# Optimization experiments

Hardware: AMD Instinct MI355X
Metric: run time of the kernel (lower is better)

Reference implementation:

```python
import jax, jax.numpy as jnp
import numpy as np

N_NODES = 100000
N_EDGES = 1600000
HID = 64
N_LAYERS = 3
BN_EPS = 1e-5


def setup_inputs() -> dict:
    key = jax.random.key(0)
    ks = jax.random.split(key, 10)
    x = jax.random.normal(ks[0], (N_NODES, HID), dtype=jnp.float32)
    edge_index = jax.random.randint(ks[1], (2, N_EDGES), 0, N_NODES, dtype=jnp.int64)
    edge_atten = jax.random.uniform(ks[2], (N_EDGES, 1), dtype=jnp.float32)
    s = 1.0 / np.sqrt(HID)
    W1 = jax.random.normal(ks[3], (N_LAYERS, HID, HID), dtype=jnp.float32) * s
    b1 = jax.random.normal(ks[4], (N_LAYERS, HID), dtype=jnp.float32) * s
    gamma = jnp.ones((N_LAYERS, HID), dtype=jnp.float32)
    beta = jnp.zeros((N_LAYERS, HID), dtype=jnp.float32)
    W2 = jax.random.normal(ks[5], (N_LAYERS, HID, HID), dtype=jnp.float32) * s
    b2 = jax.random.normal(ks[6], (N_LAYERS, HID), dtype=jnp.float32) * s
    return {"x": x, "edge_index": edge_index, "edge_atten": edge_atten,
            "W1": W1, "b1": b1, "gamma": gamma, "beta": beta, "W2": W2, "b2": b2}


def reference(x, edge_index, edge_atten, W1, b1, gamma, beta, W2, b2):
    # GIN with GINConv (eps=0): out = nn(sum_{j->i} x_j * edge_atten + x_i), then ReLU
    src = edge_index[0]  # x_j gathered from source nodes
    dst = edge_index[1]  # scatter-add into target nodes
    n = x.shape[0]
    for i in range(N_LAYERS):
        msg = x[src] * edge_atten                                   # [E, H]
        agg = jax.ops.segment_sum(msg, dst, num_segments=n)         # [N, H]
        h = agg + x                                                 # (1 + eps)*x_r, eps=0
        # MLP: Linear -> BatchNorm1d (training mode, batch stats) -> ReLU -> Linear
        h = h @ W1[i] + b1[i]
        mu = jnp.mean(h, axis=0)
        var = jnp.var(h, axis=0)
        h = (h - mu) * jax.lax.rsqrt(var + BN_EPS) * gamma[i] + beta[i]
        h = jax.nn.relu(h)
        h = h @ W2[i] + b2[i]
        x = jax.nn.relu(h)  # outer self.relu after each conv
    return x
```

## Files before the change

### kernel.cpp

```cpp
#include <hip/hip_runtime.h>

#define NN 100000
#define NE 1600000
#define HID 64
#define CH 32
#define NT (NN / 16)
#define NL 3
#define BN_EPS 1e-5f
#define BSH 7
#define BNODES 128
#define NB 782
#define GP 16
#define BIN_CHUNK 8192
#define BIN_GRID ((NE + BIN_CHUNK - 1) / BIN_CHUNK)

typedef __attribute__((ext_vector_type(8))) short short8;
typedef __attribute__((ext_vector_type(4))) float f32x4;

__device__ __forceinline__ float bf2f(unsigned short u) {
    union { unsigned int i; float f; } v; v.i = ((unsigned int)u) << 16; return v.f;
}
__device__ __forceinline__ unsigned short f2bf(float f) {
    union { float f; unsigned int i; } v; v.f = f;
    unsigned int r = v.i + 0x7FFFu + ((v.i >> 16) & 1u);
    return (unsigned short)(r >> 16);
}

__global__ void k_conv(const float* __restrict__ x, ushort* __restrict__ xc) {
    int i = blockIdx.x * blockDim.x + threadIdx.x;
    float4 v = ((const float4*)x)[i];
    int node = i >> 4, c4 = (i & 15) * 4;
    int q = c4 >> 5, m = c4 & 31;
    ushort4 o;
    o.x = f2bf(v.x); o.y = f2bf(v.y); o.z = f2bf(v.z); o.w = f2bf(v.w);
    *(ushort4*)(xc + (size_t)q * NN * CH + (size_t)node * CH + m) = o;
}

__global__ void k_wpack(const float* __restrict__ W1, const float* __restrict__ W2,
                        ushort* __restrict__ wf) {
    int s = blockIdx.x, l = threadIdx.x;
    int layer = s >> 2, kind = s & 3;
    const float* W = ((kind < 2) ? W1 : W2) + (size_t)layer * HID * HID;
    ushort* o = wf + (size_t)s * 4096;
    for (int kh = 0; kh < 2; ++kh)
        for (int t = 0; t < 4; ++t)
            for (int j = 0; j < 8; ++j) {
                int k = kh * 32 + (l >> 4) * 8 + j;
                int n = t * 16 + (l & 15);
                float f = W[k * HID + n];
                ushort hi = f2bf(f);
                o[((kh * 4 + t) * 64 + l) * 8 + j] =
                    (kind & 1) ? f2bf(f - bf2f(hi)) : hi;
            }
}

__global__ __launch_bounds__(1024) void k_histB(const int* __restrict__ dst,
                                                int* __restrict__ ghist) {
    __shared__ int lh[NB];
    int tid = threadIdx.x;
    for (int i = tid; i < NB; i += 1024) lh[i] = 0;
    __syncthreads();
    int base = blockIdx.x * BIN_CHUNK;
    int end = min(base + BIN_CHUNK, NE);
    for (int e = base + tid * 4; e + 3 < end; e += 4096) {
        int4 d = *(const int4*)(dst + e);
        atomicAdd(&lh[d.x >> BSH], 1);
        atomicAdd(&lh[d.y >> BSH], 1);
        atomicAdd(&lh[d.z >> BSH], 1);
        atomicAdd(&lh[d.w >> BSH], 1);
    }
    __syncthreads();
    for (int i = tid; i < NB; i += 1024)
        if (lh[i]) atomicAdd(&ghist[i * GP], lh[i]);
}

__global__ void k_scanB(const int* __restrict__ ghist, int* __restrict__ boffB,
                        int* __restrict__ gcur) {
    __shared__ int t[1024];
    int tid = threadIdx.x;
    int v = (tid < NB) ? ghist[tid * GP] : 0;
    t[tid] = v;
    __syncthreads();
    for (int d = 1; d < 1024; d <<= 1) {
        int u = (tid >= d) ? t[tid - d] : 0;
        __syncthreads();
        t[tid] += u;
        __syncthreads();
    }
    if (tid < NB) { int ex = t[tid] - v; boffB[tid] = ex; gcur[tid * GP] = ex; }
    if (tid == 0) boffB[NB] = NE;
}

__global__ __launch_bounds__(1024) void k_binB(const int* __restrict__ ei,
                                               const float* __restrict__ att,
                                               int* __restrict__ gcur,
                                               int2* __restrict__ evb) {
    __shared__ int lh[NB];
    int tid = threadIdx.x;
    for (int i = tid; i < NB; i += 1024) lh[i] = 0;
    __syncthreads();
    int base = blockIdx.x * BIN_CHUNK;
    int end = min(base + BIN_CHUNK, NE);
    for (int e = base + tid * 4; e + 3 < end; e += 4096) {
        int4 d = *(const int4*)(ei + NE + e);
        atomicAdd(&lh[d.x >> BSH], 1);
        atomicAdd(&lh[d.y >> BSH], 1);
        atomicAdd(&lh[d.z >> BSH], 1);
        atomicAdd(&lh[d.w >> BSH], 1);
    }
    __syncthreads();
    for (int i = tid; i < NB; i += 1024) {
        int c = lh[i];
        lh[i] = c ? atomicAdd(&gcur[i * GP], c) : 0;
    }
    __syncthreads();
    for (int e = base + tid * 4; e + 3 < end; e += 4096) {
        int4 s = *(const int4*)(ei + e);
        int4 d = *(const int4*)(ei + NE + e);
        float4 a = *(const float4*)(att + e);
        int p0 = atomicAdd(&lh[d.x >> BSH], 1);
        int p1 = atomicAdd(&lh[d.y >> BSH], 1);
        int p2 = atomicAdd(&lh[d.z >> BSH], 1);
        int p3 = atomicAdd(&lh[d.w >> BSH], 1);
        evb[p0] = make_int2(s.x | ((d.x & (BNODES - 1)) << 17), __float_as_int(a.x));
        evb[p1] = make_int2(s.y | ((d.y & (BNODES - 1)) << 17), __float_as_int(a.y));
        evb[p2] = make_int2(s.z | ((d.z & (BNODES - 1)) << 17), __float_as_int(a.z));
        evb[p3] = make_int2(s.w | ((d.w & (BNODES - 1)) << 17), __float_as_int(a.w));
    }
}

__global__ __launch_bounds__(256) void k_scatter2(const int2* __restrict__ evb,
                                                  const int* __restrict__ boffB,
                                                  int* __restrict__ offs,
                                                  uint* __restrict__ evc) {
    __shared__ int h[BNODES];
    __shared__ int cur[BNODES];
    int tid = threadIdx.x;
    int b = blockIdx.x;
    int node0 = b << BSH;
    int nvalid = min(BNODES, NN - node0);
    int e0 = boffB[b], e1 = boffB[b + 1];
    if (tid < BNODES) h[tid] = 0;
    __syncthreads();
    for (int e = e0 + tid * 2; e < e1; e += 512) {
        int2 r0 = evb[e];
        int v1 = (e + 1 < e1);
        int2 r1 = evb[v1 ? e + 1 : e];
        atomicAdd(&h[r0.x >> 17], 1);
        if (v1) atomicAdd(&h[r1.x >> 17], 1);
    }
    __syncthreads();
    int v = (tid < BNODES) ? h[tid] : 0;
    for (int d = 1; d < BNODES; d <<= 1) {
        int u = (tid >= d && tid < BNODES) ? h[tid - d] : 0;
        __syncthreads();
        if (tid < BNODES) h[tid] += u;
        __syncthreads();
    }
    if (tid < BNODES) {
        int start = e0 + h[tid] - v;
        cur[tid] = start;
        if (tid < nvalid) offs[node0 + tid] = start;
    }
    if (b == NB - 1 && tid == 0) offs[NN] = NE;
    __syncthreads();
    for (int e = e0 + tid * 2; e < e1; e += 512) {
        int2 r0 = evb[e];
        int v1 = (e + 1 < e1);
        int2 r1 = evb[v1 ? e + 1 : e];
        int p0 = atomicAdd(&cur[r0.x >> 17], 1);
        int p1 = v1 ? atomicAdd(&cur[r1.x >> 17], 1) : 0;
        uint a0 = (uint)(__int_as_float(r0.y) * 32767.0f + 0.5f);
        evc[p0] = ((uint)r0.x & 0x1FFFFu) | (a0 << 17);
        if (v1) {
            uint a1 = (uint)(__int_as_float(r1.y) * 32767.0f + 0.5f);
            evc[p1] = ((uint)r1.x & 0x1FFFFu) | (a1 << 17);
        }
    }
}

__global__ __launch_bounds__(256, 8) void k_gather(const ushort* __restrict__ xc,
                                                   const int* __restrict__ offs,
                                                   const uint* __restrict__ evc,
                                                   ushort* __restrict__ aggc) {
    int tid = threadIdx.x;
    int wv = tid >> 6, lane = tid & 63;
    int g = lane >> 4;
    int c2 = lane & 15;
    int q = (blockIdx.x & 7) >> 2;
    int wb = ((blockIdx.x >> 3) << 2) | (blockIdx.x & 3);
    const ushort* xq = xc + (size_t)q * NN * CH + c2 * 2;
    ushort* aq = aggc + (size_t)q * NN * CH;
    int slot = wb * 4 + wv;
    for (int base = slot * 8; base < NN; base += 4096 * 8) {
        uint self0 = *(const uint*)(xq + (base + g) * CH);
        uint self1 = *(const uint*)(xq + (base + g + 4) * CH);
        int myoff = offs[min(base + c2, NN)];
        float rx0 = 0.f, ry0 = 0.f, rx1 = 0.f, ry1 = 0.f;
        int e0n = __shfl(myoff, 0, 64);
        int e1n = __shfl(myoff, 1, 64);
        uint evj = evc[min(e0n + g, max(e1n - 1, 0))];
        for (int j = 0; j < 8; ++j) {
            int e0 = e0n, e1 = e1n;
            uint evu = evj;
            if (j < 7) {
                e0n = __shfl(myoff, j + 1, 64);
                e1n = __shfl(myoff, j + 2, 64);
                evj = evc[min(e0n + g, max(e1n - 1, 0))];
            }
            int e1m1 = max(e1 - 1, 0);
            float ax = 0.f, ay = 0.f;
            for (int e = e0; e < e1; e += 4) {
                uint evn = evc[min(e + 4 + g, e1m1)];
                float a = (e + g < e1) ? (float)(evu >> 17) * (1.0f / 32767.0f) : 0.f;
                uint r = *(const uint*)(xq + (evu & 0x1FFFF) * CH);
                union { uint u; float f; } lo, hi;
                lo.u = r << 16; hi.u = r & 0xFFFF0000u;
                ax += lo.f * a; ay += hi.f * a;
                evu = evn;
            }
            ax += __shfl_xor(ax, 16, 64); ax += __shfl_xor(ax, 32, 64);
            ay += __shfl_xor(ay, 16, 64); ay += __shfl_xor(ay, 32, 64);
            if (j == g)     { rx0 = ax; ry0 = ay; }
            if (j == g + 4) { rx1 = ax; ry1 = ay; }
        }
        union { uint u; float f; } s;
        s.u = self0 << 16;         rx0 += s.f;
        s.u = self0 & 0xFFFF0000u; ry0 += s.f;
        s.u = self1 << 16;         rx1 += s.f;
        s.u = self1 & 0xFFFF0000u; ry1 += s.f;
        uint o0 = ((uint)f2bf(rx0)) | (((uint)f2bf(ry0)) << 16);
        uint o1 = ((uint)f2bf(rx1)) | (((uint)f2bf(ry1)) << 16);
        *(uint*)(aq + (base + g) * CH + c2 * 2) = o0;
        *(uint*)(aq + (base + g + 4) * CH + c2 * 2) = o1;
    }
}

__global__ __launch_bounds__(256, 2) void k_mlp1(const ushort* __restrict__ aggc,
                                                 const ushort* __restrict__ wfb,
                                                 const float* __restrict__ b1,
                                                 ushort* __restrict__ h,
                                                 float* __restrict__ stats) {
    __shared__ float red1[4][64], red2[4][64];
    int tid = threadIdx.x, wv = tid >> 6, l = tid & 63;
    int lg = l >> 4, lc = l & 15;
    short8 bhi[2][4], blo[2][4];
#pragma unroll
    for (int kh = 0; kh < 2; ++kh)
#pragma unroll
        for (int t = 0; t < 4; ++t) {
            bhi[kh][t] = *(const short8*)(wfb + ((kh * 4 + t) * 64 + l) * 8);
            blo[kh][t] = *(const short8*)(wfb + 4096 + ((kh * 4 + t) * 64 + l) * 8);
        }
    f32x4 bias4[4];
#pragma unroll
    for (int t = 0; t < 4; ++t) {
        float4 bv = *(const float4*)(b1 + t * 16 + lg * 4);
        bias4[t] = (f32x4){bv.x, bv.y, bv.z, bv.w};
    }
    float s1[16], s2[16];
#pragma unroll
    for (int i = 0; i < 16; ++i) { s1[i] = 0.f; s2[i] = 0.f; }
    int gw = blockIdx.x * 4 + wv, nw = gridDim.x * 4;
    for (int tile = gw; tile < NT; tile += nw) {
        int node = tile * 16 + lc;
        const ushort* ap = aggc + (size_t)node * CH + lg * 8;
        short8 a0 = *(const short8*)ap;
        short8 a1 = *(const short8*)(ap + (size_t)NN * CH);
        f32x4 acc[4];
#pragma unroll
        for (int t = 0; t < 4; ++t) {
            acc[t] = bias4[t];
            acc[t] = __builtin_amdgcn_mfma_f32_16x16x32_bf16(bhi[0][t], a0, acc[t], 0, 0, 0);
            acc[t] = __builtin_amdgcn_mfma_f32_16x16x32_bf16(bhi[1][t], a1, acc[t], 0, 0, 0);
            acc[t] = __builtin_amdgcn_mfma_f32_16x16x32_bf16(blo[0][t], a0, acc[t], 0, 0, 0);
            acc[t] = __builtin_amdgcn_mfma_f32_16x16x32_bf16(blo[1][t], a1, acc[t], 0, 0, 0);
        }
#pragma unroll
        for (int t = 0; t < 4; ++t) {
            ushort4 o;
            float d0 = acc[t][0], d1 = acc[t][1], d2 = acc[t][2], d3 = acc[t][3];
            s1[t * 4 + 0] += d0; s2[t * 4 + 0] += d0 * d0;
            s1[t * 4 + 1] += d1; s2[t * 4 + 1] += d1 * d1;
            s1[t * 4 + 2] += d2; s2[t * 4 + 2] += d2 * d2;
            s1[t * 4 + 3] += d3; s2[t * 4 + 3] += d3 * d3;
            o.x = f2bf(d0); o.y = f2bf(d1); o.z = f2bf(d2); o.w = f2bf(d3);
            *(ushort4*)(h + (size_t)(t >> 1) * NN * CH + (size_t)node * CH
                        + (t & 1) * 16 + lg * 4) = o;
        }
    }
#pragma unroll
    for (int i = 0; i < 16; ++i) {
        s1[i] += __shfl_xor(s1[i], 1, 64); s1[i] += __shfl_xor(s1[i], 2, 64);
        s1[i] += __shfl_xor(s1[i], 4, 64); s1[i] += __shfl_xor(s1[i], 8, 64);
        s2[i] += __shfl_xor(s2[i], 1, 64); s2[i] += __shfl_xor(s2[i], 2, 64);
        s2[i] += __shfl_xor(s2[i], 4, 64); s2[i] += __shfl_xor(s2[i], 8, 64);
    }
    if (lc == 0) {
#pragma unroll
        for (int t = 0; t < 4; ++t)
#pragma unroll
            for (int r = 0; r < 4; ++r) {
                red1[wv][t * 16 + lg * 4 + r] = s1[t * 4 + r];
                red2[wv][t * 16 + lg * 4 + r] = s2[t * 4 + r];
            }
    }
    __syncthreads();
    if (tid < 64)
        atomicAdd(&stats[tid], red1[0][tid] + red1[1][tid] + red1[2][tid] + red1[3][tid]);
    else if (tid < 128) {
        int c = tid - 64;
        atomicAdd(&stats[HID + c], red2[0][c] + red2[1][c] + red2[2][c] + red2[3][c]);
    }
}

__global__ __launch_bounds__(256, 2) void k_mlp2(const ushort* __restrict__ wfb,
                                                 const float* __restrict__ b2,
                                                 const float* __restrict__ gamma,
                                                 const float* __restrict__ beta,
                                                 const float* __restrict__ stats,
                                                 const ushort* __restrict__ h,
                                                 ushort* __restrict__ xc_out,
                                                 float* __restrict__ f_out,
                                                 int write_f32) {
    int tid = threadIdx.x, wv = tid >> 6, l = tid & 63;
    int lg = l >> 4, lc = l & 15;
    short8 bhi[2][4], blo[2][4];
#pragma unroll
    for (int kh = 0; kh < 2; ++kh)
#pragma unroll
        for (int t = 0; t < 4; ++t) {
            bhi[kh][t] = *(const short8*)(wfb + 8192 + ((kh * 4 + t) * 64 + l) * 8);
            blo[kh][t] = *(const short8*)(wfb + 12288 + ((kh * 4 + t) * 64 + l) * 8);
        }
    f32x4 bias4[4];
#pragma unroll
    for (int t = 0; t < 4; ++t) {
        float4 bv = *(const float4*)(b2 + t * 16 + lg * 4);
        bias4[t] = (f32x4){bv.x, bv.y, bv.z, bv.w};
    }
    float aCk[2][8], bCk[2][8];
#pragma unroll
    for (int kh = 0; kh < 2; ++kh)
#pragma unroll
        for (int j = 0; j < 8; ++j) {
            int k = kh * 32 + lg * 8 + j;
            float mu = stats[k] * (1.0f / NN);
            float var = fmaxf(stats[HID + k] * (1.0f / NN) - mu * mu, 0.f);
            float aC = gamma[k] * rsqrtf(var + BN_EPS);
            aCk[kh][j] = aC;
            bCk[kh][j] = beta[k] - mu * aC;
        }
    int gw = blockIdx.x * 4 + wv, nw = gridDim.x * 4;
    for (int tile = gw; tile < NT; tile += nw) {
        int node = tile * 16 + lc;
        const ushort* hp = h + (size_t)node * CH + lg * 8;
        short8 a0r = *(const short8*)hp;
        short8 a1r = *(const short8*)(hp + (size_t)NN * CH);
        short8 a0, a1;
#pragma unroll
        for (int j = 0; j < 8; ++j) {
            float v0 = fmaxf(aCk[0][j] * bf2f((ushort)a0r[j]) + bCk[0][j], 0.f);
            float v1 = fmaxf(aCk[1][j] * bf2f((ushort)a1r[j]) + bCk[1][j], 0.f);
            a0[j] = (short)f2bf(v0);
            a1[j] = (short)f2bf(v1);
        }
        f32x4 acc[4];
#pragma unroll
        for (int t = 0; t < 4; ++t) {
            acc[t] = bias4[t];
            acc[t] = __builtin_amdgcn_mfma_f32_16x16x32_bf16(bhi[0][t], a0, acc[t], 0, 0, 0);
            acc[t] = __builtin_amdgcn_mfma_f32_16x16x32_bf16(bhi[1][t], a1, acc[t], 0, 0, 0);
            acc[t] = __builtin_amdgcn_mfma_f32_16x16x32_bf16(blo[0][t], a0, acc[t], 0, 0, 0);
            acc[t] = __builtin_amdgcn_mfma_f32_16x16x32_bf16(blo[1][t], a1, acc[t], 0, 0, 0);
        }
        if (write_f32) {
#pragma unroll
            for (int t = 0; t < 4; ++t) {
                float4 o4;
                o4.x = fmaxf(acc[t][0], 0.f); o4.y = fmaxf(acc[t][1], 0.f);
                o4.z = fmaxf(acc[t][2], 0.f); o4.w = fmaxf(acc[t][3], 0.f);
                *(float4*)(f_out + (size_t)node * HID + t * 16 + lg * 4) = o4;
            }
        } else {
#pragma unroll
            for (int t = 0; t < 4; ++t) {
                ushort4 o;
                o.x = f2bf(fmaxf(acc[t][0], 0.f)); o.y = f2bf(fmaxf(acc[t][1], 0.f));
                o.z = f2bf(fmaxf(acc[t][2], 0.f)); o.w = f2bf(fmaxf(acc[t][3], 0.f));
                *(ushort4*)(xc_out + (size_t)(t >> 1) * NN * CH + (size_t)node * CH
                            + (t & 1) * 16 + lg * 4) = o;
            }
        }
    }
}

extern "C" void kernel_launch(void* const* d_in, const int* in_sizes, int n_in,
                              void* d_out, int out_size, void* d_ws, size_t ws_size,
                              hipStream_t stream) {
    const float* x_in  = (const float*)d_in[0];
    const int*   ei    = (const int*)d_in[1];
    const float* att   = (const float*)d_in[2];
    const float* W1    = (const float*)d_in[3];
    const float* b1    = (const float*)d_in[4];
    const float* gamma = (const float*)d_in[5];
    const float* beta  = (const float*)d_in[6];
    const float* W2    = (const float*)d_in[7];
    const float* b2    = (const float*)d_in[8];
    float* out = (float*)d_out;

    char* ws = (char*)d_ws;
    size_t off = 0;
    auto alloc = [&](size_t bytes) -> void* {
        void* p = ws + off;
        off += (bytes + 255) & ~(size_t)255;
        return p;
    };
    ushort* xc    = (ushort*)alloc((size_t)NN * HID * 2);
    ushort* aggc  = (ushort*)alloc((size_t)NN * HID * 2);
    ushort* hb    = (ushort*)alloc((size_t)NN * HID * 2);
    ushort* wf    = (ushort*)alloc((size_t)12 * 4096 * 2);
    int*    ghist = (int*)alloc((size_t)NB * GP * 4);
    int*    boffB = (int*)alloc((size_t)(NB + 1) * 4);
    int*    gcur  = (int*)alloc((size_t)NB * GP * 4);
    int*    offs  = (int*)alloc((size_t)(NN + 1) * 4);
    int2*   evb   = (int2*)alloc((size_t)NE * 8);
    uint*   evc   = (uint*)alloc((size_t)NE * 4);
    float*  stats = (float*)alloc(NL * 128 * 4);

    hipMemsetAsync(ghist, 0, (size_t)NB * GP * 4, stream);
    hipMemsetAsync(stats, 0, NL * 128 * 4, stream);

    k_conv<<<(NN * HID / 4 + 255) / 256, 256, 0, stream>>>(x_in, xc);
    k_wpack<<<12, 64, 0, stream>>>(W1, W2, wf);
    k_histB<<<BIN_GRID, 1024, 0, stream>>>(ei + NE, ghist);
    k_scanB<<<1, 1024, 0, stream>>>(ghist, boffB, gcur);
    k_binB<<<BIN_GRID, 1024, 0, stream>>>(ei, att, gcur, evb);
    k_scatter2<<<NB, 256, 0, stream>>>(evb, boffB, offs, evc);

    for (int l = 0; l < NL; ++l) {
        const ushort* wfb = wf + (size_t)l * 4 * 4096;
        k_gather<<<2048, 256, 0, stream>>>(xc, offs, evc, aggc);
        k_mlp1<<<1024, 256, 0, stream>>>(aggc, wfb, b1 + l * HID, hb, stats + l * 128);
        k_mlp2<<<1024, 256, 0, stream>>>(wfb, b2 + l * HID,
                                         gamma + l * HID, beta + l * HID,
                                         stats + l * 128, hb,
                                         xc, out, (l == NL - 1) ? 1 : 0);
    }
}
```

Baseline: 391.1 us.

## Switch to row-major bf16 features and sub-sort edges by source range in gather

Drops the two-half channel-split feature layout in favour of plain row-major 64-channel bf16 rows, updating both MLP kernels to match. The scatter stage now also sub-buckets each destination's edges into eight source-index ranges, which gives sorted gather locality, and writes a finer offset table. The gather kernel is rewritten so each half-wave handles one full node row (32 lanes × 2 channels), three nodes per wave, with a 4-way unrolled edge loop instead of the shuffle-based 8-node scheme. This aims to improve L2 locality of the random source reads and remove shuffle overhead. The cost is a larger offset table and more per-key loop overhead for small segments.

Result: slower. 529.2 us (+35.3%).

```diff
diff --git a/kernel.cpp b/kernel.cpp
--- a/kernel.cpp
+++ b/kernel.cpp
@@ -3,16 +3,21 @@
 #define NN 100000
 #define NE 1600000
 #define HID 64
-#define CH 32
 #define NT (NN / 16)
 #define NL 3
 #define BN_EPS 1e-5f
 #define BSH 7
 #define BNODES 128
 #define NB 782
+#define NSH 8
+#define SSH 14
+#define NKEY (BNODES * NSH)
 #define GP 16
 #define BIN_CHUNK 8192
 #define BIN_GRID ((NE + BIN_CHUNK - 1) / BIN_CHUNK)
+#define GBLK 4167
+#define GW_TOT (GBLK * 4)
+#define NPAIR (NN / 2)
 
 typedef __attribute__((ext_vector_type(8))) short short8;
 typedef __attribute__((ext_vector_type(4))) float f32x4;
@@ -25,15 +30,19 @@
     unsigned int r = v.i + 0x7FFFu + ((v.i >> 16) & 1u);
     return (unsigned short)(r >> 16);
 }
-
-__global__ void k_conv(const float* __restrict__ x, ushort* __restrict__ xc) {
+__device__ __forceinline__ float lof(uint r) {
+    union { uint u; float f; } v; v.u = r << 16; return v.f;
+}
+__device__ __forceinline__ float hif(uint r) {
+    union { uint u; float f; } v; v.u = r & 0xFFFF0000u; return v.f;
+}
+
+__global__ void k_conv(const float* __restrict__ x, ushort* __restrict__ xb) {
     int i = blockIdx.x * blockDim.x + threadIdx.x;
     float4 v = ((const float4*)x)[i];
-    int node = i >> 4, c4 = (i & 15) * 4;
-    int q = c4 >> 5, m = c4 & 31;
     ushort4 o;
     o.x = f2bf(v.x); o.y = f2bf(v.y); o.z = f2bf(v.z); o.w = f2bf(v.w);
-    *(ushort4*)(xc + (size_t)q * NN * CH + (size_t)node * CH + m) = o;
+    ((ushort4*)xb)[i] = o;
 }
 
 __global__ void k_wpack(const float* __restrict__ W1, const float* __restrict__ W2,
@@ -131,109 +140,112 @@
 
 __global__ __launch_bounds__(256) void k_scatter2(const int2* __restrict__ evb,
                                                   const int* __restrict__ boffB,
-                                                  int* __restrict__ offs,
+                                                  int* __restrict__ offs2,
                                                   uint* __restrict__ evc) {
-    __shared__ int h[BNODES];
-    __shared__ int cur[BNODES];
-    int tid = threadIdx.x;
-    int b = blockIdx.x;
+    __shared__ int h[NKEY];
+    __shared__ int cur[NKEY];
+    __shared__ int tsum[256];
+    int tid = threadIdx.x, b = blockIdx.x;
     int node0 = b << BSH;
-    int nvalid = min(BNODES, NN - node0);
     int e0 = boffB[b], e1 = boffB[b + 1];
-    if (tid < BNODES) h[tid] = 0;
+    for (int i = tid; i < NKEY; i += 256) h[i] = 0;
     __syncthreads();
     for (int e = e0 + tid * 2; e < e1; e += 512) {
         int2 r0 = evb[e];
-        int v1 = (e + 1 < e1);
-        int2 r1 = evb[v1 ? e + 1 : e];
-        atomicAdd(&h[r0.x >> 17], 1);
-        if (v1) atomicAdd(&h[r1.x >> 17], 1);
-    }
-    __syncthreads();
-    int v = (tid < BNODES) ? h[tid] : 0;
-    for (int d = 1; d < BNODES; d <<= 1) {
-        int u = (tid >= d && tid < BNODES) ? h[tid - d] : 0;
+        atomicAdd(&h[((r0.x >> 17) << 3) | ((r0.x & 0x1FFFF) >> SSH)], 1);
+        if (e + 1 < e1) {
+            int2 r1 = evb[e + 1];
+            atomicAdd(&h[((r1.x >> 17) << 3) | ((r1.x & 0x1FFFF) >> SSH)], 1);
+        }
+    }
+    __syncthreads();
+    int c0 = h[tid * 4], c1 = h[tid * 4 + 1], c2 = h[tid * 4 + 2], c3 = h[tid * 4 + 3];
+    int S = c0 + c1 + c2 + c3;
+    tsum[tid] = S;
+    __syncthreads();
+    for (int d = 1; d < 256; d <<= 1) {
+        int u = (tid >= d) ? tsum[tid - d] : 0;
         __syncthreads();
-        if (tid < BNODES) h[tid] += u;
+        tsum[tid] += u;
         __syncthreads();
     }
-    if (tid < BNODES) {
-        int start = e0 + h[tid] - v;
-        cur[tid] = start;
-        if (tid < nvalid) offs[node0 + tid] = start;
-    }
-    if (b == NB - 1 && tid == 0) offs[NN] = NE;
+    int st0 = e0 + tsum[tid] - S;
+    int st1 = st0 + c0, st2 = st1 + c1, st3 = st2 + c2;
+    cur[tid * 4] = st0; cur[tid * 4 + 1] = st1;
+    cur[tid * 4 + 2] = st2; cur[tid * 4 + 3] = st3;
+    int gk = node0 * NSH + tid * 4;
+    offs2[gk] = st0; offs2[gk + 1] = st1; offs2[gk + 2] = st2; offs2[gk + 3] = st3;
+    if (b == NB - 1 && tid == 0) offs2[(size_t)NB * BNODES * NSH] = NE;
     __syncthreads();
     for (int e = e0 + tid * 2; e < e1; e += 512) {
         int2 r0 = evb[e];
-        int v1 = (e + 1 < e1);
-        int2 r1 = evb[v1 ? e + 1 : e];
-        int p0 = atomicAdd(&cur[r0.x >> 17], 1);
-        int p1 = v1 ? atomicAdd(&cur[r1.x >> 17], 1) : 0;
+        int k0 = ((r0.x >> 17) << 3) | ((r0.x & 0x1FFFF) >> SSH);
+        int p0 = atomicAdd(&cur[k0], 1);
         uint a0 = (uint)(__int_as_float(r0.y) * 32767.0f + 0.5f);
         evc[p0] = ((uint)r0.x & 0x1FFFFu) | (a0 << 17);
-        if (v1) {
+        if (e + 1 < e1) {
+            int2 r1 = evb[e + 1];
+            int k1 = ((r1.x >> 17) << 3) | ((r1.x & 0x1FFFF) >> SSH);
+            int p1 = atomicAdd(&cur[k1], 1);
             uint a1 = (uint)(__int_as_float(r1.y) * 32767.0f + 0.5f);
             evc[p1] = ((uint)r1.x & 0x1FFFFu) | (a1 << 17);
         }
     }
 }
 
-__global__ __launch_bounds__(256, 8) void k_gather(const ushort* __restrict__ xc,
-                                                   const int* __restrict__ offs,
+#define EDGE_BODY(AX, AY) \
+    for (; e + 4 <= e1; e += 4) { \
+        uint w0 = evc[e], w1 = evc[e + 1], w2 = evc[e + 2], w3 = evc[e + 3]; \
+        uint r0 = xq[(w0 & 0x1FFFF) * 32 + hl]; \
+        uint r1 = xq[(w1 & 0x1FFFF) * 32 + hl]; \
+        uint r2 = xq[(w2 & 0x1FFFF) * 32 + hl]; \
+        uint r3 = xq[(w3 & 0x1FFFF) * 32 + hl]; \
+        float a0 = (float)(w0 >> 17) * (1.0f / 32767.0f); \
+        float a1 = (float)(w1 >> 17) * (1.0f / 32767.0f); \
+        float a2 = (float)(w2 >> 17) * (1.0f / 32767.0f); \
+        float a3 = (float)(w3 >> 17) * (1.0f / 32767.0f); \
+        AX += lof(r0) * a0 + lof(r1) * a1 + lof(r2) * a2 + lof(r3) * a3; \
+        AY += hif(r0) * a0 + hif(r1) * a1 + hif(r2) * a2 + hif(r3) * a3; \
+    } \
+    for (; e < e1; ++e) { \
+        uint w = evc[e]; \
+        uint r = xq[(w & 0x1FFFF) * 32 + hl]; \
+        float a = (float)(w >> 17) * (1.0f / 32767.0f); \
+        AX += lof(r) * a; \
+        AY += hif(r) * a; \
+    }
+
+__global__ __launch_bounds__(256, 8) void k_gather(const ushort* __restrict__ xb,
+                                                   const int* __restrict__ offs2,
                                                    const uint* __restrict__ evc,
-                                                   ushort* __restrict__ aggc) {
+                                                   ushort* __restrict__ agg) {
     int tid = threadIdx.x;
-    int wv = tid >> 6, lane = tid & 63;
-    int g = lane >> 4;
-    int c2 = lane & 15;
-    int q = (blockIdx.x & 7) >> 2;
-    int wb = ((blockIdx.x >> 3) << 2) | (blockIdx.x & 3);
-    const ushort* xq = xc + (size_t)q * NN * CH + c2 * 2;
-    ushort* aq = aggc + (size_t)q * NN * CH;
-    int slot = wb * 4 + wv;
-    for (int base = slot * 8; base < NN; base += 4096 * 8) {
-        uint self0 = *(const uint*)(xq + (base + g) * CH);
-        uint self1 = *(const uint*)(xq + (base + g + 4) * CH);
-        int myoff = offs[min(base + c2, NN)];
-        float rx0 = 0.f, ry0 = 0.f, rx1 = 0.f, ry1 = 0.f;
-        int e0n = __shfl(myoff, 0, 64);
-        int e1n = __shfl(myoff, 1, 64);
-        uint evj = evc[min(e0n + g, max(e1n - 1, 0))];
-        for (int j = 0; j < 8; ++j) {
-            int e0 = e0n, e1 = e1n;
-            uint evu = evj;
-            if (j < 7) {
-                e0n = __shfl(myoff, j + 1, 64);
-                e1n = __shfl(myoff, j + 2, 64);
-                evj = evc[min(e0n + g, max(e1n - 1, 0))];
-            }
-            int e1m1 = max(e1 - 1, 0);
-            float ax = 0.f, ay = 0.f;
-            for (int e = e0; e < e1; e += 4) {
-                uint evn = evc[min(e + 4 + g, e1m1)];
-                float a = (e + g < e1) ? (float)(evu >> 17) * (1.0f / 32767.0f) : 0.f;
-                uint r = *(const uint*)(xq + (evu & 0x1FFFF) * CH);
-                union { uint u; float f; } lo, hi;
-                lo.u = r << 16; hi.u = r & 0xFFFF0000u;
-                ax += lo.f * a; ay += hi.f * a;
-                evu = evn;
-            }
-            ax += __shfl_xor(ax, 16, 64); ax += __shfl_xor(ax, 32, 64);
-            ay += __shfl_xor(ay, 16, 64); ay += __shfl_xor(ay, 32, 64);
-            if (j == g)     { rx0 = ax; ry0 = ay; }
-            if (j == g + 4) { rx1 = ax; ry1 = ay; }
-        }
-        union { uint u; float f; } s;
-        s.u = self0 << 16;         rx0 += s.f;
-        s.u = self0 & 0xFFFF0000u; ry0 += s.f;
-        s.u = self1 << 16;         rx1 += s.f;
-        s.u = self1 & 0xFFFF0000u; ry1 += s.f;
-        uint o0 = ((uint)f2bf(rx0)) | (((uint)f2bf(ry0)) << 16);
-        uint o1 = ((uint)f2bf(rx1)) | (((uint)f2bf(ry1)) << 16);
-        *(uint*)(aq + (base + g) * CH + c2 * 2) = o0;
-        *(uint*)(aq + (base + g + 4) * CH + c2 * 2) = o1;
-    }
+    int gw = blockIdx.x * 4 + (tid >> 6);
+    int lane = tid & 63;
+    int half = lane >> 5, hl = lane & 31;
+    const uint* xq = (const uint*)xb;
+    int p0 = gw, p1 = GW_TOT + gw, p2 = 2 * GW_TOT + gw;
+    bool v2 = (p2 < NPAIR);
+    int n0 = p0 * 2 + half;
+    int n1 = p1 * 2 + half;
+    int n2 = min(p2 * 2 + half, NN - 1);
+    uint sr;
+    sr = xq[n0 * 32 + hl]; float ax0 = lof(sr), ay0 = hif(sr);
+    sr = xq[n1 * 32 + hl]; float ax1 = lof(sr), ay1 = hif(sr);
+    sr = xq[n2 * 32 + hl]; float ax2 = lof(sr), ay2 = hif(sr);
+    for (int s = 0; s < NSH; ++s) {
+        int key, e0, e1, e;
+        key = n0 * NSH + s; e0 = offs2[key]; e1 = offs2[key + 1]; e = e0;
+        EDGE_BODY(ax0, ay0)
+        key = n1 * NSH + s; e0 = offs2[key]; e1 = offs2[key + 1]; e = e0;
+        EDGE_BODY(ax1, ay1)
+        key = n2 * NSH + s; e0 = offs2[key]; e1 = offs2[key + 1]; e = e0;
+        EDGE_BODY(ax2, ay2)
+    }
+    uint* ag = (uint*)agg;
+    ag[n0 * 32 + hl] = ((uint)f2bf(ax0)) | (((uint)f2bf(ay0)) << 16);
+    ag[n1 * 32 + hl] = ((uint)f2bf(ax1)) | (((uint)f2bf(ay1)) << 16);
+    if (v2) ag[n2 * 32 + hl] = ((uint)f2bf(ax2)) | (((uint)f2bf(ay2)) << 16);
 }
 
 __global__ __launch_bounds__(256, 2) void k_mlp1(const ushort* __restrict__ aggc,
@@ -264,9 +276,9 @@
     int gw = blockIdx.x * 4 + wv, nw = gridDim.x * 4;
     for (int tile = gw; tile < NT; tile += nw) {
         int node = tile * 16 + lc;
-        const ushort* ap = aggc + (size_t)node * CH + lg * 8;
+        const ushort* ap = aggc + (size_t)node * HID + lg * 8;
         short8 a0 = *(const short8*)ap;
-        short8 a1 = *(const short8*)(ap + (size_t)NN * CH);
+        short8 a1 = *(const short8*)(ap + 32);
         f32x4 acc[4];
 #pragma unroll
         for (int t = 0; t < 4; ++t) {
@@ -285,8 +297,7 @@
             s1[t * 4 + 2] += d2; s2[t * 4 + 2] += d2 * d2;
             s1[t * 4 + 3] += d3; s2[t * 4 + 3] += d3 * d3;
             o.x = f2bf(d0); o.y = f2bf(d1); o.z = f2bf(d2); o.w = f2bf(d3);
-            *(ushort4*)(h + (size_t)(t >> 1) * NN * CH + (size_t)node * CH
-                        + (t & 1) * 16 + lg * 4) = o;
+            *(ushort4*)(h + (size_t)node * HID + t * 16 + lg * 4) = o;
         }
     }
 #pragma unroll
@@ -320,7 +331,7 @@
                                                  const float* __restrict__ beta,
                                                  const float* __restrict__ stats,
                                                  const ushort* __restrict__ h,
-                                                 ushort* __restrict__ xc_out,
+                                                 ushort* __restrict__ xb_out,
                                                  float* __restrict__ f_out,
                                                  int write_f32) {
     int tid = threadIdx.x, wv = tid >> 6, l = tid & 63;
@@ -354,9 +365,9 @@
     int gw = blockIdx.x * 4 + wv, nw = gridDim.x * 4;
     for (int tile = gw; tile < NT; tile += nw) {
         int node = tile * 16 + lc;
-        const ushort* hp = h + (size_t)node * CH + lg * 8;
+        const ushort* hp = h + (size_t)node * HID + lg * 8;
         short8 a0r = *(const short8*)hp;
-        short8 a1r = *(const short8*)(hp + (size_t)NN * CH);
+        short8 a1r = *(const short8*)(hp + 32);
         short8 a0, a1;
 #pragma unroll
         for (int j = 0; j < 8; ++j) {
@@ -388,8 +399,7 @@
                 ushort4 o;
                 o.x = f2bf(fmaxf(acc[t][0], 0.f)); o.y = f2bf(fmaxf(acc[t][1], 0.f));
                 o.z = f2bf(fmaxf(acc[t][2], 0.f)); o.w = f2bf(fmaxf(acc[t][3], 0.f));
-                *(ushort4*)(xc_out + (size_t)(t >> 1) * NN * CH + (size_t)node * CH
-                            + (t & 1) * 16 + lg * 4) = o;
+                *(ushort4*)(xb_out + (size_t)node * HID + t * 16 + lg * 4) = o;
             }
         }
     }
@@ -416,14 +426,14 @@
         off += (bytes + 255) & ~(size_t)255;
         return p;
     };
-    ushort* xc    = (ushort*)alloc((size_t)NN * HID * 2);
-    ushort* aggc  = (ushort*)alloc((size_t)NN * HID * 2);
+    ushort* xb    = (ushort*)alloc((size_t)NN * HID * 2);
+    ushort* aggb  = (ushort*)alloc((size_t)NN * HID * 2);
     ushort* hb    = (ushort*)alloc((size_t)NN * HID * 2);
     ushort* wf    = (ushort*)alloc((size_t)12 * 4096 * 2);
     int*    ghist = (int*)alloc((size_t)NB * GP * 4);
     int*    boffB = (int*)alloc((size_t)(NB + 1) * 4);
     int*    gcur  = (int*)alloc((size_t)NB * GP * 4);
-    int*    offs  = (int*)alloc((size_t)(NN + 1) * 4);
+    int*    offs2 = (int*)alloc(((size_t)NB * BNODES * NSH + 16) * 4);
     int2*   evb   = (int2*)alloc((size_t)NE * 8);
     uint*   evc   = (uint*)alloc((size_t)NE * 4);
     float*  stats = (float*)alloc(NL * 128 * 4);
@@ -431,20 +441,20 @@
     hipMemsetAsync(ghist, 0, (size_t)NB * GP * 4, stream);
     hipMemsetAsync(stats, 0, NL * 128 * 4, stream);
 
-    k_conv<<<(NN * HID / 4 + 255) / 256, 256, 0, stream>>>(x_in, xc);
+    k_conv<<<(NN * HID / 4 + 255) / 256, 256, 0, stream>>>(x_in, xb);
     k_wpack<<<12, 64, 0, stream>>>(W1, W2, wf);
     k_histB<<<BIN_GRID, 1024, 0, stream>>>(ei + NE, ghist);
     k_scanB<<<1, 1024, 0, stream>>>(ghist, boffB, gcur);
     k_binB<<<BIN_GRID, 1024, 0, stream>>>(ei, att, gcur, evb);
-    k_scatter2<<<NB, 256, 0, stream>>>(evb, boffB, offs, evc);
+    k_scatter2<<<NB, 256, 0, stream>>>(evb, boffB, offs2, evc);
 
     for (int l = 0; l < NL; ++l) {
         const ushort* wfb = wf + (size_t)l * 4 * 4096;
-        k_gather<<<2048, 256, 0, stream>>>(xc, offs, evc, aggc);
-        k_mlp1<<<1024, 256, 0, stream>>>(aggc, wfb, b1 + l * HID, hb, stats + l * 128);
+        k_gather<<<GBLK, 256, 0, stream>>>(xb, offs2, evc, aggb);
+        k_mlp1<<<1024, 256, 0, stream>>>(aggb, wfb, b1 + l * HID, hb, stats + l * 128);
         k_mlp2<<<1024, 256, 0, stream>>>(wfb, b2 + l * HID,
                                          gamma + l * HID, beta + l * HID,
                                          stats + l * 128, hb,
-                                         xc, out, (l == NL - 1) ? 1 : 0);
-    }
-}
+                                         xb, out, (l == NL - 1) ? 1 : 0);
+    }
+}
```

## Sort nodes by degree and gather full 128B rows with wave-wide edge fetch

Applied to the files above, without the earlier changes.

Adds a counting sort of nodes by in-degree (histogram, scan, place) so each wave of the gather handles eight nodes of similar degree, which cuts divergence in the per-node edge loops. The feature layout changes from two 32-channel planes to a contiguous 64-channel bf16 row, and each lane now loads a uint4 (8 channels), so one neighbor costs a single 128-byte row fetch. Edge words are loaded once per 8 edges and shared across lanes with ds_bpermute. The cost is three extra setup kernels plus a perm indirection, and a fixed grid of 3125 blocks that assumes NN is a multiple of 32.

Result: faster. 332.6 us (-15.0%).

```diff
diff --git a/kernel.cpp b/kernel.cpp
--- a/kernel.cpp
+++ b/kernel.cpp
@@ -3,7 +3,6 @@
 #define NN 100000
 #define NE 1600000
 #define HID 64
-#define CH 32
 #define NT (NN / 16)
 #define NL 3
 #define BN_EPS 1e-5f
@@ -13,6 +12,9 @@
 #define GP 16
 #define BIN_CHUNK 8192
 #define BIN_GRID ((NE + BIN_CHUNK - 1) / BIN_CHUNK)
+#define GBLK 3125
+#define DCHUNK 8192
+#define DGRID ((NN + DCHUNK - 1) / DCHUNK)
 
 typedef __attribute__((ext_vector_type(8))) short short8;
 typedef __attribute__((ext_vector_type(4))) float f32x4;
@@ -25,15 +27,19 @@
     unsigned int r = v.i + 0x7FFFu + ((v.i >> 16) & 1u);
     return (unsigned short)(r >> 16);
 }
-
-__global__ void k_conv(const float* __restrict__ x, ushort* __restrict__ xc) {
+__device__ __forceinline__ float lof(uint r) {
+    union { uint u; float f; } v; v.u = r << 16; return v.f;
+}
+__device__ __forceinline__ float hif(uint r) {
+    union { uint u; float f; } v; v.u = r & 0xFFFF0000u; return v.f;
+}
+
+__global__ void k_conv(const float* __restrict__ x, ushort* __restrict__ xb) {
     int i = blockIdx.x * blockDim.x + threadIdx.x;
     float4 v = ((const float4*)x)[i];
-    int node = i >> 4, c4 = (i & 15) * 4;
-    int q = c4 >> 5, m = c4 & 31;
     ushort4 o;
     o.x = f2bf(v.x); o.y = f2bf(v.y); o.z = f2bf(v.z); o.w = f2bf(v.w);
-    *(ushort4*)(xc + (size_t)q * NN * CH + (size_t)node * CH + m) = o;
+    ((ushort4*)xb)[i] = o;
 }
 
 __global__ void k_wpack(const float* __restrict__ W1, const float* __restrict__ W2,
@@ -179,61 +185,108 @@
     }
 }
 
-__global__ __launch_bounds__(256, 8) void k_gather(const ushort* __restrict__ xc,
+__global__ __launch_bounds__(1024) void k_dhist(const int* __restrict__ offs,
+                                                int* __restrict__ dh) {
+    __shared__ int lh[256];
+    int tid = threadIdx.x;
+    if (tid < 256) lh[tid] = 0;
+    __syncthreads();
+    int lo = blockIdx.x * DCHUNK, hi = min(lo + DCHUNK, NN);
+    for (int i = lo + tid; i < hi; i += 1024)
+        atomicAdd(&lh[min(offs[i + 1] - offs[i], 255)], 1);
+    __syncthreads();
+    if (tid < 256 && lh[tid]) atomicAdd(&dh[tid * GP], lh[tid]);
+}
+
+__global__ void k_dscan(const int* __restrict__ dh, int* __restrict__ dcur) {
+    __shared__ int t[256];
+    int tid = threadIdx.x;
+    int v = dh[tid * GP];
+    t[tid] = v;
+    __syncthreads();
+    for (int d = 1; d < 256; d <<= 1) {
+        int u = (tid >= d) ? t[tid - d] : 0;
+        __syncthreads();
+        t[tid] += u;
+        __syncthreads();
+    }
+    dcur[tid * GP] = t[tid] - v;
+}
+
+__global__ __launch_bounds__(1024) void k_dplace(const int* __restrict__ offs,
+                                                 int* __restrict__ dcur,
+                                                 int* __restrict__ perm) {
+    __shared__ int lh[256];
+    __shared__ int lbase[256];
+    int tid = threadIdx.x;
+    if (tid < 256) lh[tid] = 0;
+    __syncthreads();
+    int lo = blockIdx.x * DCHUNK, hi = min(lo + DCHUNK, NN);
+    int mybin[8], myrk[8];
+#pragma unroll 8
+    for (int u = 0; u < 8; ++u) {
+        int i = lo + u * 1024 + tid;
+        if (i < hi) {
+            int b = min(offs[i + 1] - offs[i], 255);
+            mybin[u] = b;
+            myrk[u] = atomicAdd(&lh[b], 1);
+        } else mybin[u] = -1;
+    }
+    __syncthreads();
+    if (tid < 256) {
+        int c = lh[tid];
+        lbase[tid] = c ? atomicAdd(&dcur[tid * GP], c) : 0;
+    }
+    __syncthreads();
+#pragma unroll 8
+    for (int u = 0; u < 8; ++u) {
+        int i = lo + u * 1024 + tid;
+        if (mybin[u] >= 0) perm[lbase[mybin[u]] + myrk[u]] = i;
+    }
+}
+
+__global__ __launch_bounds__(256, 4) void k_gather(const ushort* __restrict__ xb,
                                                    const int* __restrict__ offs,
                                                    const uint* __restrict__ evc,
-                                                   ushort* __restrict__ aggc) {
-    int tid = threadIdx.x;
-    int wv = tid >> 6, lane = tid & 63;
-    int g = lane >> 4;
-    int c2 = lane & 15;
-    int q = (blockIdx.x & 7) >> 2;
-    int wb = ((blockIdx.x >> 3) << 2) | (blockIdx.x & 3);
-    const ushort* xq = xc + (size_t)q * NN * CH + c2 * 2;
-    ushort* aq = aggc + (size_t)q * NN * CH;
-    int slot = wb * 4 + wv;
-    for (int base = slot * 8; base < NN; base += 4096 * 8) {
-        uint self0 = *(const uint*)(xq + (base + g) * CH);
-        uint self1 = *(const uint*)(xq + (base + g + 4) * CH);
-        int myoff = offs[min(base + c2, NN)];
-        float rx0 = 0.f, ry0 = 0.f, rx1 = 0.f, ry1 = 0.f;
-        int e0n = __shfl(myoff, 0, 64);
-        int e1n = __shfl(myoff, 1, 64);
-        uint evj = evc[min(e0n + g, max(e1n - 1, 0))];
+                                                   const int* __restrict__ perm,
+                                                   ushort* __restrict__ agg) {
+    int tid = threadIdx.x;
+    int wid = blockIdx.x * 4 + (tid >> 6);
+    int lane = tid & 63;
+    int g = lane >> 3, k = lane & 7;
+    const uint4* xq4 = (const uint4*)xb;
+    uint4* aq4 = (uint4*)agg;
+    int node = perm[wid * 8 + g];
+    int e0 = offs[node], e1 = offs[node + 1];
+    int deg = e1 - e0;
+    uint4 s4 = xq4[(size_t)node * 8 + k];
+    float ax0 = lof(s4.x), ay0 = hif(s4.x);
+    float ax1 = lof(s4.y), ay1 = hif(s4.y);
+    float ax2 = lof(s4.z), ay2 = hif(s4.z);
+    float ax3 = lof(s4.w), ay3 = hif(s4.w);
+    int maxd = deg;
+    maxd = max(maxd, __shfl_xor(maxd, 8, 64));
+    maxd = max(maxd, __shfl_xor(maxd, 16, 64));
+    maxd = max(maxd, __shfl_xor(maxd, 32, 64));
+    for (int base = 0; base < maxd; base += 8) {
+        uint ew = evc[min(e0 + base + k, NE - 1)];
+#pragma unroll 8
         for (int j = 0; j < 8; ++j) {
-            int e0 = e0n, e1 = e1n;
-            uint evu = evj;
-            if (j < 7) {
-                e0n = __shfl(myoff, j + 1, 64);
-                e1n = __shfl(myoff, j + 2, 64);
-                evj = evc[min(e0n + g, max(e1n - 1, 0))];
-            }
-            int e1m1 = max(e1 - 1, 0);
-            float ax = 0.f, ay = 0.f;
-            for (int e = e0; e < e1; e += 4) {
-                uint evn = evc[min(e + 4 + g, e1m1)];
-                float a = (e + g < e1) ? (float)(evu >> 17) * (1.0f / 32767.0f) : 0.f;
-                uint r = *(const uint*)(xq + (evu & 0x1FFFF) * CH);
-                union { uint u; float f; } lo, hi;
-                lo.u = r << 16; hi.u = r & 0xFFFF0000u;
-                ax += lo.f * a; ay += hi.f * a;
-                evu = evn;
-            }
-            ax += __shfl_xor(ax, 16, 64); ax += __shfl_xor(ax, 32, 64);
-            ay += __shfl_xor(ay, 16, 64); ay += __shfl_xor(ay, 32, 64);
-            if (j == g)     { rx0 = ax; ry0 = ay; }
-            if (j == g + 4) { rx1 = ax; ry1 = ay; }
-        }
-        union { uint u; float f; } s;
-        s.u = self0 << 16;         rx0 += s.f;
-        s.u = self0 & 0xFFFF0000u; ry0 += s.f;
-        s.u = self1 << 16;         rx1 += s.f;
-        s.u = self1 & 0xFFFF0000u; ry1 += s.f;
-        uint o0 = ((uint)f2bf(rx0)) | (((uint)f2bf(ry0)) << 16);
-        uint o1 = ((uint)f2bf(rx1)) | (((uint)f2bf(ry1)) << 16);
-        *(uint*)(aq + (base + g) * CH + c2 * 2) = o0;
-        *(uint*)(aq + (base + g + 4) * CH + c2 * 2) = o1;
-    }
+            uint w = (uint)__builtin_amdgcn_ds_bpermute((g * 8 + j) << 2, (int)ew);
+            float a = (base + j < deg) ? (float)(w >> 17) * (1.0f / 32767.0f) : 0.f;
+            uint4 r = xq4[(size_t)(w & 0x1FFFF) * 8 + k];
+            ax0 += lof(r.x) * a; ay0 += hif(r.x) * a;
+            ax1 += lof(r.y) * a; ay1 += hif(r.y) * a;
+            ax2 += lof(r.z) * a; ay2 += hif(r.z) * a;
+            ax3 += lof(r.w) * a; ay3 += hif(r.w) * a;
+        }
+    }
+    uint4 o;
+    o.x = ((uint)f2bf(ax0)) | (((uint)f2bf(ay0)) << 16);
+    o.y = ((uint)f2bf(ax1)) | (((uint)f2bf(ay1)) << 16);
+    o.z = ((uint)f2bf(ax2)) | (((uint)f2bf(ay2)) << 16);
+    o.w = ((uint)f2bf(ax3)) | (((uint)f2bf(ay3)) << 16);
+    aq4[(size_t)node * 8 + k] = o;
 }
 
 __global__ __launch_bounds__(256, 2) void k_mlp1(const ushort* __restrict__ aggc,
@@ -264,9 +317,9 @@
     int gw = blockIdx.x * 4 + wv, nw = gridDim.x * 4;
     for (int tile = gw; tile < NT; tile += nw) {
         int node = tile * 16 + lc;
-        const ushort* ap = aggc + (size_t)node * CH + lg * 8;
+        const ushort* ap = aggc + (size_t)node * HID + lg * 8;
         short8 a0 = *(const short8*)ap;
-        short8 a1 = *(const short8*)(ap + (size_t)NN * CH);
+        short8 a1 = *(const short8*)(ap + 32);
         f32x4 acc[4];
 #pragma unroll
         for (int t = 0; t < 4; ++t) {
@@ -285,8 +338,7 @@
             s1[t * 4 + 2] += d2; s2[t * 4 + 2] += d2 * d2;
             s1[t * 4 + 3] += d3; s2[t * 4 + 3] += d3 * d3;
             o.x = f2bf(d0); o.y = f2bf(d1); o.z = f2bf(d2); o.w = f2bf(d3);
-            *(ushort4*)(h + (size_t)(t >> 1) * NN * CH + (size_t)node * CH
-                        + (t & 1) * 16 + lg * 4) = o;
+            *(ushort4*)(h + (size_t)node * HID + t * 16 + lg * 4) = o;
         }
     }
 #pragma unroll
@@ -320,7 +372,7 @@
                                                  const float* __restrict__ beta,
                                                  const float* __restrict__ stats,
                                                  const ushort* __restrict__ h,
-                                                 ushort* __restrict__ xc_out,
+                                                 ushort* __restrict__ xb_out,
                                                  float* __restrict__ f_out,
                                                  int write_f32) {
     int tid = threadIdx.x, wv = tid >> 6, l = tid & 63;
@@ -354,9 +406,9 @@
     int gw = blockIdx.x * 4 + wv, nw = gridDim.x * 4;
     for (int tile = gw; tile < NT; tile += nw) {
         int node = tile * 16 + lc;
-        const ushort* hp = h + (size_t)node * CH + lg * 8;
+        const ushort* hp = h + (size_t)node * HID + lg * 8;
         short8 a0r = *(const short8*)hp;
-        short8 a1r = *(const short8*)(hp + (size_t)NN * CH);
+        short8 a1r = *(const short8*)(hp + 32);
         short8 a0, a1;
 #pragma unroll
         for (int j = 0; j < 8; ++j) {
@@ -388,8 +440,7 @@
                 ushort4 o;
                 o.x = f2bf(fmaxf(acc[t][0], 0.f)); o.y = f2bf(fmaxf(acc[t][1], 0.f));
                 o.z = f2bf(fmaxf(acc[t][2], 0.f)); o.w = f2bf(fmaxf(acc[t][3], 0.f));
-                *(ushort4*)(xc_out + (size_t)(t >> 1) * NN * CH + (size_t)node * CH
-                            + (t & 1) * 16 + lg * 4) = o;
+                *(ushort4*)(xb_out + (size_t)node * HID + t * 16 + lg * 4) = o;
             }
         }
     }
@@ -416,8 +467,8 @@
         off += (bytes + 255) & ~(size_t)255;
         return p;
     };
-    ushort* xc    = (ushort*)alloc((size_t)NN * HID * 2);
-    ushort* aggc  = (ushort*)alloc((size_t)NN * HID * 2);
+    ushort* xb    = (ushort*)alloc((size_t)NN * HID * 2);
+    ushort* aggb  = (ushort*)alloc((size_t)NN * HID * 2);
     ushort* hb    = (ushort*)alloc((size_t)NN * HID * 2);
     ushort* wf    = (ushort*)alloc((size_t)12 * 4096 * 2);
     int*    ghist = (int*)alloc((size_t)NB * GP * 4);
@@ -426,25 +477,32 @@
     int*    offs  = (int*)alloc((size_t)(NN + 1) * 4);
     int2*   evb   = (int2*)alloc((size_t)NE * 8);
     uint*   evc   = (uint*)alloc((size_t)NE * 4);
+    int*    dh    = (int*)alloc((size_t)256 * GP * 4);
+    int*    dcur  = (int*)alloc((size_t)256 * GP * 4);
+    int*    perm  = (int*)alloc((size_t)NN * 4);
     float*  stats = (float*)alloc(NL * 128 * 4);
 
     hipMemsetAsync(ghist, 0, (size_t)NB * GP * 4, stream);
+    hipMemsetAsync(dh, 0, (size_t)256 * GP * 4, stream);
     hipMemsetAsync(stats, 0, NL * 128 * 4, stream);
 
-    k_conv<<<(NN * HID / 4 + 255) / 256, 256, 0, stream>>>(x_in, xc);
+    k_conv<<<(NN * HID / 4 + 255) / 256, 256, 0, stream>>>(x_in, xb);
     k_wpack<<<12, 64, 0, stream>>>(W1, W2, wf);
     k_histB<<<BIN_GRID, 1024, 0, stream>>>(ei + NE, ghist);
     k_scanB<<<1, 1024, 0, stream>>>(ghist, boffB, gcur);
     k_binB<<<BIN_GRID, 1024, 0, stream>>>(ei, att, gcur, evb);
     k_scatter2<<<NB, 256, 0, stream>>>(evb, boffB, offs, evc);
+    k_dhist<<<DGRID, 1024, 0, stream>>>(offs, dh);
+    k_dscan<<<1, 256, 0, stream>>>(dh, dcur);
+    k_dplace<<<DGRID, 1024, 0, stream>>>(offs, dcur, perm);
 
     for (int l = 0; l < NL; ++l) {
         const ushort* wfb = wf + (size_t)l * 4 * 4096;
-        k_gather<<<2048, 256, 0, stream>>>(xc, offs, evc, aggc);
-        k_mlp1<<<1024, 256, 0, stream>>>(aggc, wfb, b1 + l * HID, hb, stats + l * 128);
+        k_gather<<<GBLK, 256, 0, stream>>>(xb, offs, evc, perm, aggb);
+        k_mlp1<<<1024, 256, 0, stream>>>(aggb, wfb, b1 + l * HID, hb, stats + l * 128);
         k_mlp2<<<1024, 256, 0, stream>>>(wfb, b2 + l * HID,
                                          gamma + l * HID, beta + l * HID,
                                          stats + l * 128, hb,
-                                         xc, out, (l == NL - 1) ? 1 : 0);
-    }
-}
+                                         xb, out, (l == NL - 1) ? 1 : 0);
+    }
+}
```
